# Optimization experiments

Measured on AMD Instinct MI355X. Metric: run time of the kernel, lower is better.

Reference implementation:

```python
import jax, jax.numpy as jnp
import numpy as np

N = 50000      # nodes
E = 800000     # edges (avg degree 16)
DIN = 128
H = 128
DOUT = 64


def setup_inputs() -> dict:
    key = jax.random.key(0)
    ks = jax.random.split(key, 8)
    x = jax.random.normal(ks[0], (N, DIN), dtype=jnp.float32)
    edge_index = jax.random.randint(ks[1], (2, E), 0, N, dtype=jnp.int32)
    def glorot(k, fi, fo):
        return jax.random.normal(k, (fi, fo), dtype=jnp.float32) * (1.0 / np.sqrt(fi))
    return {
        "x": x,
        "edge_index": edge_index,
        "W1": glorot(ks[2], DIN, H), "b1": jnp.zeros((H,), jnp.float32),
        "W2": glorot(ks[3], H, H),   "b2": jnp.zeros((H,), jnp.float32),
        "W3": glorot(ks[4], H, DOUT),"b3": jnp.zeros((DOUT,), jnp.float32),
    }


def reference(x, edge_index, W1, b1, W2, b2, W3, b3):
    n = x.shape[0]
    # GCNConv: add self-loops, symmetric degree normalization D^-1/2 (A+I) D^-1/2
    loop = jnp.arange(n, dtype=edge_index.dtype)
    src = jnp.concatenate([edge_index[0], loop])  # [E+N]
    dst = jnp.concatenate([edge_index[1], loop])
    deg = jax.ops.segment_sum(jnp.ones(src.shape, x.dtype), dst, num_segments=n)
    dinv = jnp.where(deg > 0, jax.lax.rsqrt(deg), 0.0)
    norm = dinv[src] * dinv[dst]  # [E+N]

    def conv(h, W, b):
        h = h @ W                                   # [N, out]
        msg = h[src] * norm[:, None]                # gather + scale
        return jax.ops.segment_sum(msg, dst, num_segments=n) + b

    # gelu after every layer except the last (forward breaks before act)
    h = jax.nn.gelu(conv(x, W1, b1), approximate=False)
    h = jax.nn.gelu(conv(h, W2, b2), approximate=False)
    return conv(h, W3, b3)
```

## Files before the change

kernel.cpp:

```cpp
#include <hip/hip_runtime.h>
#include <math.h>

#define NDIN 128
#define NHID 128
#define NDOUT 64

typedef _Float16 half2_t __attribute__((ext_vector_type(2)));
typedef _Float16 half4_t __attribute__((ext_vector_type(4)));
typedef _Float16 half8_t __attribute__((ext_vector_type(8)));
typedef float    float4v __attribute__((ext_vector_type(4)));

__device__ __forceinline__ float gelu_exact(float x) {
    return 0.5f * x * (1.0f + erff(x * 0.70710678118654752f));
}


__device__ void wtrans_tile(const float* __restrict__ W, _Float16* __restrict__ Wt,
                            int K, int N, int bx, int by) {
    __shared__ float tile[32][33];
    int tx = threadIdx.x & 31, ty = threadIdx.x >> 5;
    for (int i = 0; i < 32; i += 8) {
        int k = by * 32 + ty + i, nn = bx * 32 + tx;
        tile[ty + i][tx] = (k < K && nn < N) ? W[(size_t)k * N + nn] : 0.f;
    }
    __syncthreads();
    for (int i = 0; i < 32; i += 8) {
        int nn = bx * 32 + ty + i, k = by * 32 + tx;
        if (nn < N && k < K) Wt[(size_t)nn * K + k] = (_Float16)tile[tx][ty + i];
    }
}

__global__ __launch_bounds__(256) void prep0_kernel(
    const float* __restrict__ W1, _Float16* __restrict__ W1t,
    const float* __restrict__ W2, _Float16* __restrict__ W2t,
    const float* __restrict__ W3, _Float16* __restrict__ W3t,
    int* __restrict__ count, int* __restrict__ done, int n) {
    int b = blockIdx.x;
    if (b < 16) {
        wtrans_tile(W1, W1t, NDIN, NHID, b & 3, b >> 2);
    } else if (b < 32) {
        wtrans_tile(W2, W2t, NHID, NHID, (b - 16) & 3, (b - 16) >> 2);
    } else if (b < 40) {
        wtrans_tile(W3, W3t, NHID, NDOUT, (b - 32) & 1, (b - 32) >> 1);
    } else {
        int z = b - 40;
        int i = z * 256 + threadIdx.x;
        if (i < n) count[i] = 0;
        if (z == 0 && threadIdx.x < 64) done[threadIdx.x] = 0;
    }
}


__global__ void count_kernel(const int* __restrict__ dst, int* __restrict__ count,
                             int* __restrict__ eslot, int E) {
    int e = blockIdx.x * blockDim.x + threadIdx.x;
    if (e < E) eslot[e] = atomicAdd(&count[dst[e]], 1);
}


__global__ __launch_bounds__(256) void reduce_scan_kernel(
    const int* __restrict__ count, int* __restrict__ blocksum, int* __restrict__ blockoff,
    int* __restrict__ rowptr, float* __restrict__ dinv, int* __restrict__ done,
    int nb, int n) {
    __shared__ int s[256];
    __shared__ int flag;
    __shared__ int boff_s;
    int t = threadIdx.x;
    int i = blockIdx.x * 256 + t;
    int v = (i < n) ? count[i] : 0;
    s[t] = v;
    __syncthreads();
    for (int off = 128; off > 0; off >>= 1) {
        if (t < off) s[t] += s[t + off];
        __syncthreads();
    }
    if (t == 0) {
        atomicExch(&blocksum[blockIdx.x], s[0]);
        __threadfence();
        int old = atomicAdd(&done[0], 1);
        flag = (old == nb - 1) ? 1 : 0;
    }
    __syncthreads();
    if (flag) {
        __threadfence();
        int pv = (t < nb) ? atomicAdd(&blocksum[t], 0) : 0;
        s[t] = pv;
        __syncthreads();
        for (int off = 1; off < 256; off <<= 1) {
            int u = (t >= off) ? s[t - off] : 0;
            __syncthreads();
            s[t] += u;
            __syncthreads();
        }
        if (t < nb) atomicExch(&blockoff[t], s[t] - pv);
        if (t == 255) rowptr[n] = s[255];
        __threadfence();
        if (t == 0) atomicExch(&done[1], 1);
    } else if (t == 0) {
        while (atomicAdd(&done[1], 0) == 0) __builtin_amdgcn_s_sleep(2);
        __threadfence();
    }
    __syncthreads();
    if (t == 0) boff_s = atomicAdd(&blockoff[blockIdx.x], 0);
    s[t] = v;
    __syncthreads();
    for (int off = 1; off < 256; off <<= 1) {
        int u = (t >= off) ? s[t - off] : 0;
        __syncthreads();
        s[t] += u;
        __syncthreads();
    }
    if (i < n) {
        rowptr[i] = boff_s + s[t] - v;
        dinv[i] = rsqrtf((float)(v + 1));
    }
}


__global__ void fill_kernel(const int* __restrict__ src, const int* __restrict__ dst,
                            const int* __restrict__ eslot, const float* __restrict__ dinv,
                            const int* __restrict__ rowptr, int2* __restrict__ adj, int E) {
    int e = blockIdx.x * blockDim.x + threadIdx.x;
    if (e >= E) return;
    int s = src[e], d = dst[e];
    int p = rowptr[d] + eslot[e];
    adj[p] = make_int2(s, __float_as_int(dinv[s] * dinv[d]));
}


template <int BN, bool AF16>
__global__ __launch_bounds__(256) void gemm_mfma(
    const void* __restrict__ Aptr, const _Float16* __restrict__ Bt,
    _Float16* __restrict__ T, int M) {
    __shared__ _Float16 lds_a[64][136];
    __shared__ _Float16 lds_bt[BN][136];
    const int K = 128;
    int tid = threadIdx.x;
    int bm = blockIdx.x * 64;
    int wave = tid >> 6, lane = tid & 63;
    int m = lane & 15, quad = lane >> 4;

    if (AF16) {
        const _Float16* A = (const _Float16*)Aptr;
#pragma unroll
        for (int j = 0; j < 4; j++) {
            int c = tid + j * 256;
            int r = c >> 4, col = (c & 15) << 3;
            int grow = bm + r;
            uint4 v = make_uint4(0, 0, 0, 0);
            if (grow < M) v = *(const uint4*)(A + (size_t)grow * K + col);
            *(uint4*)&lds_a[r][col] = v;
        }
    } else {
        const float* A = (const float*)Aptr;
#pragma unroll
        for (int j = 0; j < 8; j++) {
            int c = tid + j * 256;
            int r = c >> 5, col = (c & 31) << 2;
            int grow = bm + r;
            float4 v = make_float4(0.f, 0.f, 0.f, 0.f);
            if (grow < M) v = *(const float4*)(A + (size_t)grow * K + col);
            half4_t h;
            h[0] = (_Float16)v.x; h[1] = (_Float16)v.y;
            h[2] = (_Float16)v.z; h[3] = (_Float16)v.w;
            *(half4_t*)&lds_a[r][col] = h;
        }
    }
    {
        const int chunks = BN * K / 8;
        for (int c = tid; c < chunks; c += 256) {
            int r = c >> 4, col = (c & 15) << 3;
            *(uint4*)&lds_bt[r][col] = *(const uint4*)(Bt + (size_t)r * K + col);
        }
    }
    __syncthreads();

    const int NT = BN / 16;
    float4v acc[NT];
#pragma unroll
    for (int nt = 0; nt < NT; nt++) acc[nt] = (float4v){0.f, 0.f, 0.f, 0.f};

    int arow = (wave << 4) + m;
#pragma unroll
    for (int kc = 0; kc < K; kc += 32) {
        half8_t a = *(const half8_t*)&lds_a[arow][kc + quad * 8];
#pragma unroll
        for (int nt = 0; nt < NT; nt++) {
            half8_t b = *(const half8_t*)&lds_bt[nt * 16 + m][kc + quad * 8];
            acc[nt] = __builtin_amdgcn_mfma_f32_16x16x32_f16(a, b, acc[nt], 0, 0, 0);
        }
    }
#pragma unroll
    for (int nt = 0; nt < NT; nt++) {
#pragma unroll
        for (int r = 0; r < 4; r++) {
            int grow = bm + (wave << 4) + (quad << 2) + r;
            if (grow < M) T[(size_t)grow * BN + nt * 16 + m] = (_Float16)acc[nt][r];
        }
    }
}


__device__ __forceinline__ half2_t agg_node128(
    const half2_t* __restrict__ t2, const int* __restrict__ rowptr,
    const int2* __restrict__ adj, const float* __restrict__ dinv,
    const float* __restrict__ bias, int node, int lane) {
    float wself = dinv[node];
    wself *= wself;
    half2_t v = t2[(size_t)node * 64 + lane];
    float accx = wself * (float)v[0], accy = wself * (float)v[1];
    int beg = rowptr[node], end = rowptr[node + 1];
    for (int e0 = beg; e0 < end; e0 += 64) {
        int rem = end - e0;
        int j = 0; float w = 0.f;
        if (lane < rem) {
            int2 ed = adj[e0 + lane];
            j = ed.x; w = __int_as_float(ed.y);
        }
        int cnt = rem < 64 ? rem : 64;
        for (int c = 0; c < cnt; c += 16) {
#pragma unroll
            for (int i = 0; i < 16; i++) {
                int jj = __builtin_amdgcn_readlane(j, c + i);
                float ww = __int_as_float(
                    __builtin_amdgcn_readlane(__float_as_int(w), c + i));
                half2_t u = t2[(size_t)jj * 64 + lane];
                accx += ww * (float)u[0];
                accy += ww * (float)u[1];
            }
        }
    }
    float2 b = ((const float2*)bias)[lane];
    accx = gelu_exact(accx + b.x);
    accy = gelu_exact(accy + b.y);
    half2_t o; o[0] = (_Float16)accx; o[1] = (_Float16)accy;
    return o;
}


template <int BN>
__global__ __launch_bounds__(256) void agg_gemm16_kernel(
    const _Float16* __restrict__ t, const int* __restrict__ rowptr,
    const int2* __restrict__ adj, const float* __restrict__ dinv,
    const float* __restrict__ bias, const _Float16* __restrict__ Bt,
    _Float16* __restrict__ T, int M) {
    __shared__ _Float16 lds_a[16][136];
    int tid = threadIdx.x;
    int wave = tid >> 6, lane = tid & 63;
    int bm = blockIdx.x * 16;
    const half2_t* t2 = (const half2_t*)t;
#pragma unroll 1
    for (int p = 0; p < 4; p++) {
        int r = (wave << 2) + p;
        int node = bm + r;
        half2_t o;
        o[0] = (_Float16)0.f; o[1] = (_Float16)0.f;
        if (node < M) o = agg_node128(t2, rowptr, adj, dinv, bias, node, lane);
        *(half2_t*)&lds_a[r][lane << 1] = o;
    }
    __syncthreads();

    int m = lane & 15, quad = lane >> 4;
    const int NT = BN / 64;
    float4v acc[NT];
#pragma unroll
    for (int nt = 0; nt < NT; nt++) acc[nt] = (float4v){0.f, 0.f, 0.f, 0.f};
#pragma unroll
    for (int kc = 0; kc < 128; kc += 32) {
        half8_t a = *(const half8_t*)&lds_a[m][kc + quad * 8];
#pragma unroll
        for (int nt = 0; nt < NT; nt++) {
            int col = wave * (BN / 4) + nt * 16 + m;
            half8_t b = *(const half8_t*)&Bt[(size_t)col * 128 + kc + quad * 8];
            acc[nt] = __builtin_amdgcn_mfma_f32_16x16x32_f16(a, b, acc[nt], 0, 0, 0);
        }
    }
#pragma unroll
    for (int nt = 0; nt < NT; nt++) {
#pragma unroll
        for (int r = 0; r < 4; r++) {
            int grow = bm + (quad << 2) + r;
            int col = wave * (BN / 4) + nt * 16 + m;
            if (grow < M) T[(size_t)grow * BN + col] = (_Float16)acc[nt][r];
        }
    }
}


template <int F, bool DOGELU, bool OUTF16>
__global__ __launch_bounds__(256) void agg_kernel(
    const _Float16* __restrict__ t, const int* __restrict__ rowptr,
    const int2* __restrict__ adj, const float* __restrict__ dinv,
    const float* __restrict__ bias, void* __restrict__ outp, int n) {
    int node = (int)((blockIdx.x * blockDim.x + threadIdx.x) >> 6);
    int lane = threadIdx.x & 63;
    if (node >= n) return;

    float wself = dinv[node];
    wself *= wself;
    int beg = rowptr[node];
    int end = rowptr[node + 1];

    if (F == 128) {
        const half2_t* t2 = (const half2_t*)t;
        half2_t v = t2[(size_t)node * 64 + lane];
        float accx = wself * (float)v[0], accy = wself * (float)v[1];
        for (int e0 = beg; e0 < end; e0 += 64) {
            int rem = end - e0;
            int j = 0; float w = 0.f;
            if (lane < rem) {
                int2 ed = adj[e0 + lane];
                j = ed.x; w = __int_as_float(ed.y);
            }
            int cnt = rem < 64 ? rem : 64;
            for (int c = 0; c < cnt; c += 16) {
#pragma unroll
                for (int i = 0; i < 16; i++) {
                    int jj = __builtin_amdgcn_readlane(j, c + i);
                    float ww = __int_as_float(
                        __builtin_amdgcn_readlane(__float_as_int(w), c + i));
                    half2_t u = t2[(size_t)jj * 64 + lane];
                    accx += ww * (float)u[0];
                    accy += ww * (float)u[1];
                }
            }
        }
        float2 b = ((const float2*)bias)[lane];
        accx += b.x; accy += b.y;
        if (DOGELU) { accx = gelu_exact(accx); accy = gelu_exact(accy); }
        if (OUTF16) {
            half2_t o; o[0] = (_Float16)accx; o[1] = (_Float16)accy;
            ((half2_t*)outp)[(size_t)node * 64 + lane] = o;
        } else {
            float2 o; o.x = accx; o.y = accy;
            ((float2*)outp)[(size_t)node * 64 + lane] = o;
        }
    } else {
        float acc = wself * (float)t[(size_t)node * 64 + lane];
        for (int e0 = beg; e0 < end; e0 += 64) {
            int rem = end - e0;
            int j = 0; float w = 0.f;
            if (lane < rem) {
                int2 ed = adj[e0 + lane];
                j = ed.x; w = __int_as_float(ed.y);
            }
            int cnt = rem < 64 ? rem : 64;
            for (int c = 0; c < cnt; c += 16) {
#pragma unroll
                for (int i = 0; i < 16; i++) {
                    int jj = __builtin_amdgcn_readlane(j, c + i);
                    float ww = __int_as_float(
                        __builtin_amdgcn_readlane(__float_as_int(w), c + i));
                    acc += ww * (float)t[(size_t)jj * 64 + lane];
                }
            }
        }
        acc += bias[lane];
        if (DOGELU) acc = gelu_exact(acc);
        if (OUTF16) ((_Float16*)outp)[(size_t)node * 64 + lane] = (_Float16)acc;
        else        ((float*)outp)[(size_t)node * 64 + lane] = acc;
    }
}


extern "C" void kernel_launch(void* const* d_in, const int* in_sizes, int n_in,
                              void* d_out, int out_size, void* d_ws, size_t ws_size,
                              hipStream_t stream) {
    const float* x  = (const float*)d_in[0];
    const int* edge = (const int*)d_in[1];
    const float* W1 = (const float*)d_in[2];
    const float* b1 = (const float*)d_in[3];
    const float* W2 = (const float*)d_in[4];
    const float* b2 = (const float*)d_in[5];
    const float* W3 = (const float*)d_in[6];
    const float* b3 = (const float*)d_in[7];
    float* out = (float*)d_out;

    const int N = in_sizes[0] / NDIN;
    const int E = in_sizes[1] / 2;
    const int* src = edge;
    const int* dst = edge + E;
    const int NB = (N + 255) / 256;

    char* p = (char*)d_ws;
    auto alloc = [&](size_t bytes) {
        char* q = p;
        p += (bytes + 255) & ~(size_t)255;
        return q;
    };
    int*       count    = (int*)alloc((size_t)N * 4);
    int*       rowptr   = (int*)alloc((size_t)(N + 1) * 4);
    int*       blocksum = (int*)alloc((size_t)NB * 4);
    int*       blockoff = (int*)alloc((size_t)NB * 4);
    int*       done     = (int*)alloc(256);
    float*     dinv     = (float*)alloc((size_t)N * 4);
    int*       eslot    = (int*)alloc((size_t)E * 4);
    int2*      adj      = (int2*)alloc((size_t)E * 8);
    _Float16*  W1t      = (_Float16*)alloc((size_t)NHID * NDIN * 2);
    _Float16*  W2t      = (_Float16*)alloc((size_t)NHID * NHID * 2);
    _Float16*  W3t      = (_Float16*)alloc((size_t)NDOUT * NHID * 2);
    _Float16*  tbuf     = (_Float16*)alloc((size_t)N * NHID * 2);
    _Float16*  hbuf     = (_Float16*)alloc((size_t)N * NHID * 2);

    dim3 blk(256);
    int mtiles = (N + 63) / 64;
    int ntiles16 = (N + 15) / 16;
    int eblocks = (E + 255) / 256;
    int agg_blocks = (N + 3) / 4;

    prep0_kernel<<<40 + NB, blk, 0, stream>>>(W1, W1t, W2, W2t, W3, W3t, count, done, N);
    count_kernel<<<eblocks, blk, 0, stream>>>(dst, count, eslot, E);
    reduce_scan_kernel<<<NB, blk, 0, stream>>>(count, blocksum, blockoff, rowptr,
                                               dinv, done, NB, N);
    fill_kernel<<<eblocks, blk, 0, stream>>>(src, dst, eslot, dinv, rowptr, adj, E);
    gemm_mfma<128, false><<<mtiles, blk, 0, stream>>>(x, W1t, tbuf, N);
    agg_gemm16_kernel<128><<<ntiles16, blk, 0, stream>>>(tbuf, rowptr, adj, dinv, b1,
                                                         W2t, hbuf, N);
    agg_kernel<128, true, true><<<agg_blocks, blk, 0, stream>>>(hbuf, rowptr, adj,
                                                                dinv, b2, tbuf, N);
    gemm_mfma<64, true><<<mtiles, blk, 0, stream>>>(tbuf, W3t, hbuf, N);
    agg_kernel<64, false, false><<<agg_blocks, blk, 0, stream>>>(hbuf, rowptr, adj,
                                                                 dinv, b3, out, N);
}
```

Before: 268.1 us.

## Use one wave per node in fused agg-GEMM and fuse layer-2 aggregation with W3 GEMM

```diff
diff --git a/kernel.cpp b/kernel.cpp
--- a/kernel.cpp
+++ b/kernel.cpp
@@ -239,7 +239,7 @@
 
 
 template <int BN>
-__global__ __launch_bounds__(256) void agg_gemm16_kernel(
+__global__ __launch_bounds__(1024) void agg_gemm16w_kernel(
     const _Float16* __restrict__ t, const int* __restrict__ rowptr,
     const int2* __restrict__ adj, const float* __restrict__ dinv,
     const float* __restrict__ bias, const _Float16* __restrict__ Bt,
@@ -249,39 +249,28 @@
     int wave = tid >> 6, lane = tid & 63;
     int bm = blockIdx.x * 16;
     const half2_t* t2 = (const half2_t*)t;
-#pragma unroll 1
-    for (int p = 0; p < 4; p++) {
-        int r = (wave << 2) + p;
-        int node = bm + r;
-        half2_t o;
-        o[0] = (_Float16)0.f; o[1] = (_Float16)0.f;
-        if (node < M) o = agg_node128(t2, rowptr, adj, dinv, bias, node, lane);
-        *(half2_t*)&lds_a[r][lane << 1] = o;
-    }
-    __syncthreads();
-
-    int m = lane & 15, quad = lane >> 4;
-    const int NT = BN / 64;
-    float4v acc[NT];
-#pragma unroll
-    for (int nt = 0; nt < NT; nt++) acc[nt] = (float4v){0.f, 0.f, 0.f, 0.f};
-#pragma unroll
-    for (int kc = 0; kc < 128; kc += 32) {
-        half8_t a = *(const half8_t*)&lds_a[m][kc + quad * 8];
-#pragma unroll
-        for (int nt = 0; nt < NT; nt++) {
-            int col = wave * (BN / 4) + nt * 16 + m;
-            half8_t b = *(const half8_t*)&Bt[(size_t)col * 128 + kc + quad * 8];
-            acc[nt] = __builtin_amdgcn_mfma_f32_16x16x32_f16(a, b, acc[nt], 0, 0, 0);
-        }
-    }
-#pragma unroll
-    for (int nt = 0; nt < NT; nt++) {
+
+    int node = bm + wave;
+    half2_t o;
+    o[0] = (_Float16)0.f; o[1] = (_Float16)0.f;
+    if (node < M) o = agg_node128(t2, rowptr, adj, dinv, bias, node, lane);
+    *(half2_t*)&lds_a[wave][lane << 1] = o;
+    __syncthreads();
+
+    const int NCT = BN / 16;
+    if (wave < NCT) {
+        int m = lane & 15, quad = lane >> 4;
+        float4v acc = (float4v){0.f, 0.f, 0.f, 0.f};
+#pragma unroll
+        for (int kc = 0; kc < 128; kc += 32) {
+            half8_t a = *(const half8_t*)&lds_a[m][kc + quad * 8];
+            half8_t b = *(const half8_t*)&Bt[(size_t)(wave * 16 + m) * 128 + kc + quad * 8];
+            acc = __builtin_amdgcn_mfma_f32_16x16x32_f16(a, b, acc, 0, 0, 0);
+        }
 #pragma unroll
         for (int r = 0; r < 4; r++) {
             int grow = bm + (quad << 2) + r;
-            int col = wave * (BN / 4) + nt * 16 + m;
-            if (grow < M) T[(size_t)grow * BN + col] = (_Float16)acc[nt][r];
+            if (grow < M) T[(size_t)grow * BN + wave * 16 + m] = (_Float16)acc[r];
         }
     }
 }
@@ -403,6 +392,7 @@
     _Float16*  hbuf     = (_Float16*)alloc((size_t)N * NHID * 2);
 
     dim3 blk(256);
+    dim3 blk1k(1024);
     int mtiles = (N + 63) / 64;
     int ntiles16 = (N + 15) / 16;
     int eblocks = (E + 255) / 256;
@@ -414,11 +404,10 @@
                                                dinv, done, NB, N);
     fill_kernel<<<eblocks, blk, 0, stream>>>(src, dst, eslot, dinv, rowptr, adj, E);
     gemm_mfma<128, false><<<mtiles, blk, 0, stream>>>(x, W1t, tbuf, N);
-    agg_gemm16_kernel<128><<<ntiles16, blk, 0, stream>>>(tbuf, rowptr, adj, dinv, b1,
-                                                         W2t, hbuf, N);
-    agg_kernel<128, true, true><<<agg_blocks, blk, 0, stream>>>(hbuf, rowptr, adj,
-                                                                dinv, b2, tbuf, N);
-    gemm_mfma<64, true><<<mtiles, blk, 0, stream>>>(tbuf, W3t, hbuf, N);
-    agg_kernel<64, false, false><<<agg_blocks, blk, 0, stream>>>(hbuf, rowptr, adj,
+    agg_gemm16w_kernel<128><<<ntiles16, blk1k, 0, stream>>>(tbuf, rowptr, adj, dinv, b1,
+                                                            W2t, hbuf, N);
+    agg_gemm16w_kernel<64><<<ntiles16, blk1k, 0, stream>>>(hbuf, rowptr, adj, dinv, b2,
+                                                           W3t, tbuf, N);
+    agg_kernel<64, false, false><<<agg_blocks, blk, 0, stream>>>(tbuf, rowptr, adj,
                                                                  dinv, b3, out, N);
 }
```

Result: no change. 268.8 us (+0.2%).
